# Performance work log

Measured on AMD Instinct MI355X. Metric: run time of the kernel, lower is better.

Reference implementation:

```python
import jax, jax.numpy as jnp
import numpy as np

EPS = 1.1920929e-07  # torch RMSNorm default eps = finfo(fp32).eps
NUM_HEADS = 8
UP_HEAD = 64
ROPE_HEAD = 32
TOP_K = 4
HIDDEN = 512
INTER = 256
DQ = 256
DKV = 128
N_EXPERTS = 16
B, S = 2, 2048


def _rmsnorm(x, w):
    return x * jax.lax.rsqrt(jnp.mean(x * x, axis=-1, keepdims=True) + EPS) * w


def _rope(x):
    # x: [B, h, S, D] with D = ROPE_HEAD; rotate-half RoPE, base 10000
    D = x.shape[-1]
    s = x.shape[-2]
    inv_freq = 1.0 / (10000.0 ** (jnp.arange(0, D, 2, dtype=jnp.float32) / D))
    freqs = jnp.outer(jnp.arange(s, dtype=jnp.float32), inv_freq)  # [S, D/2]
    emb = jnp.concatenate([freqs, freqs], axis=-1)  # [S, D]
    cos, sin = jnp.cos(emb), jnp.sin(emb)
    x1, x2 = x[..., : D // 2], x[..., D // 2:]
    rot = jnp.concatenate([-x2, x1], axis=-1)
    return x * cos + rot * sin


def _swiglu(x, wg, wu, wd):
    return (jax.nn.silu(x @ wg) * (x @ wu)) @ wd


def setup_inputs() -> dict:
    key = jax.random.key(0)
    ks = jax.random.split(key, 18)
    sd = 0.02
    inp = {
        "hidden_states": jax.random.normal(ks[0], (B, S, HIDDEN), jnp.float32),
        "w_in_norm": jnp.ones((HIDDEN,), jnp.float32),
        "w_dq": sd * jax.random.normal(ks[1], (HIDDEN, DQ), jnp.float32),
        "w_qnorm": jnp.ones((DQ,), jnp.float32),
        "w_uq": sd * jax.random.normal(ks[2], (DQ, NUM_HEADS * (UP_HEAD + ROPE_HEAD)), jnp.float32),
        "w_dkv": sd * jax.random.normal(ks[3], (HIDDEN, DKV + ROPE_HEAD), jnp.float32),
        "w_kvnorm": jnp.ones((DKV,), jnp.float32),
        "w_ukv": sd * jax.random.normal(ks[4], (DKV, NUM_HEADS * UP_HEAD * 2), jnp.float32),
        "w_o": sd * jax.random.normal(ks[5], (NUM_HEADS * UP_HEAD, HIDDEN), jnp.float32),
        "w_post_norm": jnp.ones((HIDDEN,), jnp.float32),
        "w_gate": sd * jax.random.normal(ks[6], (HIDDEN, N_EXPERTS), jnp.float32),
        "sh_wg": sd * jax.random.normal(ks[7], (HIDDEN, INTER), jnp.float32),
        "sh_wu": sd * jax.random.normal(ks[8], (HIDDEN, INTER), jnp.float32),
        "sh_wd": sd * jax.random.normal(ks[9], (INTER, HIDDEN), jnp.float32),
        "r_wg": sd * jax.random.normal(ks[10], (N_EXPERTS, HIDDEN, INTER), jnp.float32),
        "r_wu": sd * jax.random.normal(ks[11], (N_EXPERTS, HIDDEN, INTER), jnp.float32),
        "r_wd": sd * jax.random.normal(ks[12], (N_EXPERTS, INTER, HIDDEN), jnp.float32),
    }
    return inp


def reference(hidden_states, w_in_norm, w_dq, w_qnorm, w_uq, w_dkv, w_kvnorm,
              w_ukv, w_o, w_post_norm, w_gate, sh_wg, sh_wu, sh_wd,
              r_wg, r_wu, r_wd):
    b, s, h = hidden_states.shape
    # ---- MLA attention block ----
    residual = hidden_states
    x = _rmsnorm(hidden_states, w_in_norm)
    c_q = x @ w_dq                                             # [B,S,Dq]
    qcr = _rmsnorm(c_q, w_qnorm) @ w_uq                        # [B,S,nh*(uh+rh)]
    qcr = qcr.reshape(b, s, NUM_HEADS, UP_HEAD + ROPE_HEAD).transpose(0, 2, 1, 3)
    q_c, q_r = qcr[..., :UP_HEAD], qcr[..., UP_HEAD:]
    ckv_kr = x @ w_dkv                                         # [B,S,Dkv+rh]
    c_kv, k_r = ckv_kr[..., :DKV], ckv_kr[..., DKV:]
    k_r = k_r[:, None, :, :]                                   # [B,1,S,rh]
    kv = (_rmsnorm(c_kv, w_kvnorm) @ w_ukv).reshape(b, s, NUM_HEADS, 2 * UP_HEAD).transpose(0, 2, 1, 3)
    k_c, v = kv[..., :UP_HEAD], kv[..., UP_HEAD:]
    q = jnp.concatenate([q_c, _rope(q_r)], axis=-1)            # [B,nh,S,96]
    k = jnp.concatenate([k_c, jnp.broadcast_to(_rope(k_r), (b, NUM_HEADS, s, ROPE_HEAD))], axis=-1)
    scale = 1.0 / jnp.sqrt(jnp.float32(UP_HEAD + ROPE_HEAD))
    attn = jax.nn.softmax(jnp.einsum('bhqd,bhkd->bhqk', q, k) * scale, axis=-1)
    o = jnp.einsum('bhqk,bhkd->bhqd', attn, v).transpose(0, 2, 1, 3).reshape(b, s, NUM_HEADS * UP_HEAD)
    x = o @ w_o + residual
    # ---- MoE block ----
    residual = x
    x = _rmsnorm(x, w_post_norm)
    x2 = x.reshape(-1, h)                                      # [T,H]
    shared = _swiglu(x2, sh_wg, sh_wu, sh_wd)                  # [T,H]
    scores = jax.nn.sigmoid(x2 @ w_gate)                       # [T,E]
    tw, ti = jax.lax.top_k(scores, TOP_K)                      # [T,k]
    tw = tw / jnp.sum(tw, axis=-1, keepdims=True)
    # combine[t,e] = routing weight of expert e for token t (0 if not selected)
    combine = jnp.sum(jax.nn.one_hot(ti, N_EXPERTS, dtype=x2.dtype) * tw[..., None], axis=1)  # [T,E]
    g = jnp.einsum('th,ehi->tei', x2, r_wg)
    u = jnp.einsum('th,ehi->tei', x2, r_wu)
    y = jnp.einsum('tei,eih->teh', jax.nn.silu(g) * u, r_wd)   # per-expert SwiGLU outputs
    routed = jnp.einsum('teh,te->th', y, combine)
    return (shared + routed).reshape(b, s, h) + residual
```

## Files before the change

kernel.cpp:

```cpp
#include <hip/hip_runtime.h>
#include <hip/hip_bf16.h>
#include <math.h>

typedef float f32x4 __attribute__((ext_vector_type(4)));
typedef short s16x8 __attribute__((ext_vector_type(8)));

constexpr int Tt = 4096;
constexpr int NEn = 16;
constexpr float EPSf = 1.1920929e-07f;

__device__ __forceinline__ short f2b(float f) {
    union { __hip_bfloat16 h; short s; } u;
    u.h = __float2bfloat16(f);
    return u.s;
}
__device__ __forceinline__ float b2f(short s) {
    union { float f; unsigned u; } v;
    v.u = ((unsigned)(unsigned short)s) << 16;
    return v.f;
}

constexpr size_t alg(size_t x) { return (x + 15) & ~(size_t)15; }
constexpr size_t OFF_CQKV = 0;
constexpr size_t OFF_QCR  = alg(OFF_CQKV + (size_t)Tt * 416);
constexpr size_t OFF_KVB  = alg(OFF_QCR  + (size_t)Tt * 768);
constexpr size_t OFF_R2   = alg(OFF_KVB  + (size_t)Tt * 1024);
constexpr size_t OFF_TOKE = alg(OFF_R2   + (size_t)Tt * 512);
constexpr size_t OFF_TOKW = alg(OFF_TOKE + (size_t)Tt * 4);
constexpr size_t OFF_EWT  = alg(OFF_TOKW + (size_t)Tt * 4);
constexpr size_t OFF_ECNT = alg(OFF_EWT  + (size_t)NEn * Tt);
constexpr size_t OFF_ETOK = alg(OFF_ECNT + 64);
constexpr size_t OFF_PO   = 0;
constexpr size_t OFF_PL   = (size_t)16 * 2048 * 4 * 64 / 2;
constexpr size_t OFF_XNB   = alg(OFF_ETOK + (size_t)NEn * Tt);
constexpr size_t OFF_CQNB  = alg(OFF_XNB   + (size_t)Tt * 512 / 2);
constexpr size_t OFF_CKVNB = alg(OFF_CQNB  + (size_t)Tt * 256 / 2);
constexpr size_t OFF_QB    = alg(OFF_CKVNB + (size_t)Tt * 128 / 2);
constexpr size_t OFF_KB    = alg(OFF_QB    + (size_t)16 * 2048 * 96 / 2);
constexpr size_t OFF_VBT   = alg(OFF_KB    + (size_t)16 * 2048 * 96 / 2);
constexpr size_t OFF_XN2B  = alg(OFF_VBT   + (size_t)16 * 64 * 2048 / 2);
constexpr size_t OFF_GACT  = alg(OFF_XN2B  + (size_t)Tt * 512 / 2);
constexpr size_t OFF_EACT  = alg(OFF_GACT  + (size_t)Tt * 256 / 2);
constexpr size_t OFF_WQKVT = alg(OFF_EACT  + (size_t)16384 * 256 / 2);
constexpr size_t OFF_WUQT  = alg(OFF_WQKVT + (size_t)416 * 512 / 2);
constexpr size_t OFF_WUKVT = alg(OFF_WUQT  + (size_t)768 * 256 / 2);
constexpr size_t OFF_WOT   = alg(OFF_WUKVT + (size_t)1024 * 128 / 2);
constexpr size_t OFF_SHWGT = alg(OFF_WOT   + (size_t)512 * 512 / 2);
constexpr size_t OFF_SHWUT = alg(OFF_SHWGT + (size_t)256 * 512 / 2);
constexpr size_t OFF_SHWDT = alg(OFF_SHWUT + (size_t)256 * 512 / 2);
constexpr size_t OFF_RWGT  = alg(OFF_SHWDT + (size_t)512 * 256 / 2);
constexpr size_t OFF_RWUT  = alg(OFF_RWGT  + (size_t)16 * 256 * 512 / 2);
constexpr size_t OFF_RWDT  = alg(OFF_RWUT  + (size_t)16 * 256 * 512 / 2);

struct CvtTab {
    const float* src[11];
    short* dst[11];
    int K[11], N[11], end[11];
};
__global__ __launch_bounds__(256)
void k_cvt_all(CvtTab tab) {
    __shared__ float t[32][33];
    int bid = blockIdx.x;
    int i = 0;
    while (bid >= tab.end[i]) ++i;
    int tloc = bid - (i ? tab.end[i - 1] : 0);
    int K = tab.K[i], N = tab.N[i];
    int ntiles = N >> 5, perE = ntiles * (K >> 5);
    int e = tloc / perE, rem = tloc - e * perE;
    int k0 = (rem / ntiles) << 5, n0 = (rem % ntiles) << 5;
    size_t eo = (size_t)e * K * N;
    const float* src = tab.src[i];
    short* dst = tab.dst[i];
    int c = threadIdx.x & 31, r = threadIdx.x >> 5;
#pragma unroll
    for (int q = 0; q < 4; ++q)
        t[r + 8 * q][c] = src[eo + (size_t)(k0 + r + 8 * q) * N + n0 + c];
    __syncthreads();
#pragma unroll
    for (int q = 0; q < 4; ++q)
        dst[eo + (size_t)(n0 + r + 8 * q) * K + k0 + c] = f2b(t[c][r + 8 * q]);
}

__global__ void k_rms(const float* __restrict__ in, int inStride, const float* __restrict__ w,
                      short* __restrict__ outB, int outStride, int D, int* __restrict__ ecnt) {
    int row = blockIdx.x, tid = threadIdx.x;
    if (row == 0 && tid < 16) ecnt[tid] = 0;
    __shared__ float xs[512];
    __shared__ float red[256];
    const float* ip = in + (size_t)row * inStride;
    float ss = 0.f;
    for (int i = tid; i < D; i += 256) { float v = ip[i]; xs[i] = v; ss += v * v; }
    red[tid] = ss; __syncthreads();
    for (int s = 128; s > 0; s >>= 1) { if (tid < s) red[tid] += red[tid + s]; __syncthreads(); }
    float sc = rsqrtf(red[0] / (float)D + EPSf);
    for (int i = tid; i < D; i += 256) outB[(size_t)row * outStride + i] = f2b(xs[i] * sc * w[i]);
}

__global__ void k_rms2(const float* __restrict__ cqkv, const float* __restrict__ wq, short* __restrict__ cqnb,
                       const float* __restrict__ wkv, short* __restrict__ ckvnb) {
    int row = blockIdx.x, tid = threadIdx.x;
    __shared__ float xs[256];
    __shared__ float red[256];
    const float* ip; const float* w; short* ob; int D, outStride, r;
    if (row < Tt) { r = row;      ip = cqkv + (size_t)r * 416;       w = wq;  ob = cqnb;  D = 256; outStride = 256; }
    else          { r = row - Tt; ip = cqkv + (size_t)r * 416 + 256; w = wkv; ob = ckvnb; D = 128; outStride = 128; }
    float ss = 0.f;
    for (int i = tid; i < D; i += 256) { float v = ip[i]; xs[i] = v; ss += v * v; }
    red[tid] = ss; __syncthreads();
    for (int s = 128; s > 0; s >>= 1) { if (tid < s) red[tid] += red[tid + s]; __syncthreads(); }
    float sc = rsqrtf(red[0] / (float)D + EPSf);
    for (int i = tid; i < D; i += 256) ob[(size_t)r * outStride + i] = f2b(xs[i] * sc * w[i]);
}

__global__ __launch_bounds__(256)
void k_rms_router(const float* __restrict__ r2, const float* __restrict__ wpost,
                  const float* __restrict__ wg,
                  short* __restrict__ xn2b, int4* __restrict__ toke, float4* __restrict__ tokw) {
    int t = blockIdx.x, tid = threadIdx.x;
    __shared__ float xs[512];
    __shared__ float red[256];
    __shared__ float part[16][17];
    __shared__ float sc[16];
    const float* ip = r2 + (size_t)t * 512;
    float ss = 0.f;
    for (int i = tid; i < 512; i += 256) { float v = ip[i]; xs[i] = v; ss += v * v; }
    red[tid] = ss; __syncthreads();
    for (int s = 128; s > 0; s >>= 1) { if (tid < s) red[tid] += red[tid + s]; __syncthreads(); }
    float scale = rsqrtf(red[0] / 512.f + EPSf);
// ... 15 lines not shown
    if (tid < 16) {
        float s = 0.f;
#pragma unroll
        for (int c = 0; c < 16; ++c) s += part[c][tid];
        sc[tid] = 1.f / (1.f + expf(-s));
    }
    __syncthreads();
    if (tid < 64) {
        int lane = tid, e = lane & 15;
        float scv = sc[e];
        unsigned sel = 0;
        float tw[4]; int ti[4];
#pragma unroll
        for (int kk = 0; kk < 4; ++kk) {
            float cand = ((sel >> e) & 1u) ? -1e30f : scv;
            float mx = cand;
            mx = fmaxf(mx, __shfl_xor(mx, 1));
            mx = fmaxf(mx, __shfl_xor(mx, 2));
            mx = fmaxf(mx, __shfl_xor(mx, 4));
            mx = fmaxf(mx, __shfl_xor(mx, 8));
            unsigned long long msk = __ballot(cand == mx);
            int bi = (__ffsll(msk) - 1) & 15;
            tw[kk] = mx; ti[kk] = bi;
            sel |= 1u << bi;
        }
        if (lane == 0) {
            float inv = 1.f / (tw[0] + tw[1] + tw[2] + tw[3]);
            toke[t] = make_int4(ti[0], ti[1], ti[2], ti[3]);
            tokw[t] = make_float4(tw[0] * inv, tw[1] * inv, tw[2] * inv, tw[3] * inv);
        }
    }
}

template <int EPI>
__global__ __launch_bounds__(512)
void k_mgemm(const short* __restrict__ A, const short* __restrict__ BT,
             void* __restrict__ Cv, const float* __restrict__ add, int N, int K,
             short* __restrict__ aux, short* __restrict__ aux2) {
    __shared__ __align__(16) short As[64 * 64];
    __shared__ __align__(16) short Bs[64 * 64];
    int tid = threadIdx.x;
    int w = tid >> 6, l = tid & 63, g = l >> 4, li = l & 15;
    int wm = w >> 1, wn = w & 1;
    int m0 = blockIdx.y * 64, n0 = blockIdx.x * 64;
    f32x4 acc[2] = {};
    for (int k0 = 0; k0 < K; k0 += 64) {
        __syncthreads();
        {
            int row = tid >> 3, ch = tid & 7;
            *(int4*)&As[row * 64 + ((ch ^ (row & 7)) * 8)] =
                *(const int4*)(A + (size_t)(m0 + row) * K + k0 + 8 * ch);
            int4 v = {0, 0, 0, 0};
            if (n0 + row < N) v = *(const int4*)(BT + (size_t)(n0 + row) * K + k0 + 8 * ch);
            *(int4*)&Bs[row * 64 + ((ch ^ (row & 7)) * 8)] = v;
        }
        __syncthreads();
#pragma unroll
        for (int kc = 0; kc < 2; ++kc) {
            int row = wm * 16 + li;
            s16x8 af = *(const s16x8*)&As[row * 64 + (((4 * kc + g) ^ (li & 7)) * 8)];
#pragma unroll
            for (int nt = 0; nt < 2; ++nt) {
                int n = wn * 32 + nt * 16 + li;
                s16x8 bf = *(const s16x8*)&Bs[n * 64 + (((4 * kc + g) ^ (li & 7)) * 8)];
                acc[nt] = __builtin_amdgcn_mfma_f32_16x16x32_bf16(af, bf, acc[nt], 0, 0, 0);
            }
        }
    }
#pragma unroll
    for (int nt = 0; nt < 2; ++nt)
#pragma unroll
        for (int r = 0; r < 4; ++r) {
            int gm = m0 + wm * 16 + 4 * g + r;
            int gn = n0 + wn * 32 + nt * 16 + li;
            if (gn < N) {
                float v = acc[nt][r];
                if (EPI == 1) {
                    ((float*)Cv)[(size_t)gm * N + gn] = v + add[(size_t)gm * N + gn];
                } else if (EPI == 2) {
                    ((short*)Cv)[(size_t)gm * N + gn] = f2b(v);
                } else if (EPI == 3) {
                    int h = gn >> 7, dd = gn & 127;
                    int b = gm >> 11, srow = gm & 2047;
                    int bh = b * 8 + h;
                    if (dd < 64)
                        aux[((size_t)(bh * 2048 + srow)) * 96 + dd] = f2b(v);
                    else
                        aux2[(size_t)bh * 64 * 2048 + (size_t)(dd - 64) * 2048 + srow] = f2b(v);
                } else if (EPI == 4) {
                    int h = gn / 96, dd = gn - h * 96;
                    int b = gm >> 11, srow = gm & 2047;
                    int bh = b * 8 + h;
                    if (dd < 64)
                        aux[((size_t)(bh * 2048 + srow)) * 96 + dd] = f2b(v * 0.14724389f);
                    else
                        ((short*)Cv)[(size_t)gm * N + gn] = f2b(v);
                } else {
                    ((float*)Cv)[(size_t)gm * N + gn] = v;
                }
            }
        }
}

__global__ __launch_bounds__(512)
void k_wo_gemm(const short* __restrict__ po, const float* __restrict__ pl,
               const short* __restrict__ BT, float* __restrict__ C,
               const float* __restrict__ add) {
    constexpr int N = 512, K = 512;
    __shared__ __align__(16) short As[64 * 64];
    __shared__ __align__(16) short Bs[64 * 64];
    int tid = threadIdx.x;
    int w = tid >> 6, l = tid & 63, g = l >> 4, li = l & 15;
    int wm = w >> 1, wn = w & 1;
    int m0 = blockIdx.y * 64, n0 = blockIdx.x * 64;
    int row = tid >> 3, ch = tid & 7;
    int t = m0 + row;
    int b = t >> 11, q = t & 2047;
    f32x4 acc[2] = {};
    for (int k0 = 0; k0 < K; k0 += 64) {
        int h = k0 >> 6;
        int bhq = (b * 8 + h) * 2048 + q;
        size_t pb = (size_t)bhq * 256 + 8 * ch;
        float4 l4 = *(const float4*)(pl + (size_t)bhq * 4);
        float inv = 1.f / (l4.x + l4.y + l4.z + l4.w);
        union { int4 v; short s[8]; } p0, p1, p2, p3, ov;
        p0.v = *(const int4*)(po + pb);
        p1.v = *(const int4*)(po + pb + 64);
        p2.v = *(const int4*)(po + pb + 128);
        p3.v = *(const int4*)(po + pb + 192);
#pragma unroll
        for (int i = 0; i < 8; ++i) {
            float os = b2f(p0.s[i]) + b2f(p1.s[i]) + b2f(p2.s[i]) + b2f(p3.s[i]);
            ov.s[i] = f2b(os * inv);
        }
        int4 bv = *(const int4*)(BT + (size_t)(n0 + row) * K + k0 + 8 * ch);
        __syncthreads();
        *(int4*)&As[row * 64 + ((ch ^ (row & 7)) * 8)] = ov.v;
        *(int4*)&Bs[row * 64 + ((ch ^ (row & 7)) * 8)] = bv;
        __syncthreads();
#pragma unroll
        for (int kc = 0; kc < 2; ++kc) {
            int rr = wm * 16 + li;
            s16x8 af = *(const s16x8*)&As[rr * 64 + (((4 * kc + g) ^ (li & 7)) * 8)];
#pragma unroll
            for (int nt = 0; nt < 2; ++nt) {
                int n = wn * 32 + nt * 16 + li;
                s16x8 bf = *(const s16x8*)&Bs[n * 64 + (((4 * kc + g) ^ (li & 7)) * 8)];
                acc[nt] = __builtin_amdgcn_mfma_f32_16x16x32_bf16(af, bf, acc[nt], 0, 0, 0);
            }
        }
    }
#pragma unroll
    for (int nt = 0; nt < 2; ++nt)
#pragma unroll
        for (int r = 0; r < 4; ++r) {
            int gm = m0 + wm * 16 + 4 * g + r;
            int gn = n0 + wn * 32 + nt * 16 + li;
            C[(size_t)gm * N + gn] = acc[nt][r] + add[(size_t)gm * N + gn];
        }
}

__global__ __launch_bounds__(512)
void k_shexp(const short* __restrict__ X, const short* __restrict__ WGt, const short* __restrict__ WUt,
             short* __restrict__ gact) {
    __shared__ __align__(16) short As[64 * 64];
    __shared__ __align__(16) short Bg[64 * 64];
    __shared__ __align__(16) short Bu[64 * 64];
    int tid = threadIdx.x;
    int w = tid >> 6, l = tid & 63, g = l >> 4, li = l & 15;
    int wm = w >> 1, wn = w & 1;
    int m0 = blockIdx.x * 64, n0 = blockIdx.y * 64;
    f32x4 ag[2] = {}, au[2] = {};
    for (int k0 = 0; k0 < 512; k0 += 64) {
        __syncthreads();
        {
            int row = tid >> 3, ch = tid & 7;
            *(int4*)&As[row * 64 + ((ch ^ (row & 7)) * 8)] =
                *(const int4*)(X + (size_t)(m0 + row) * 512 + k0 + 8 * ch);
            *(int4*)&Bg[row * 64 + ((ch ^ (row & 7)) * 8)] =
                *(const int4*)(WGt + (size_t)(n0 + row) * 512 + k0 + 8 * ch);
            *(int4*)&Bu[row * 64 + ((ch ^ (row & 7)) * 8)] =
                *(const int4*)(WUt + (size_t)(n0 + row) * 512 + k0 + 8 * ch);
        }
        __syncthreads();
#pragma unroll
        for (int kc = 0; kc < 2; ++kc) {
            int row = wm * 16 + li;
            s16x8 af = *(const s16x8*)&As[row * 64 + (((4 * kc + g) ^ (li & 7)) * 8)];
#pragma unroll
            for (int nt = 0; nt < 2; ++nt) {
                int n = wn * 32 + nt * 16 + li;
                s16x8 bg = *(const s16x8*)&Bg[n * 64 + (((4 * kc + g) ^ (li & 7)) * 8)];
                s16x8 bu = *(const s16x8*)&Bu[n * 64 + (((4 * kc + g) ^ (li & 7)) * 8)];
                ag[nt] = __builtin_amdgcn_mfma_f32_16x16x32_bf16(af, bg, ag[nt], 0, 0, 0);
                au[nt] = __builtin_amdgcn_mfma_f32_16x16x32_bf16(af, bu, au[nt], 0, 0, 0);
            }
        }
    }
#pragma unroll
    for (int nt = 0; nt < 2; ++nt)
#pragma unroll
        for (int r = 0; r < 4; ++r) {
            int gm = m0 + wm * 16 + 4 * g + r;
            int gn = n0 + wn * 32 + nt * 16 + li;
            float gv = ag[nt][r], uv = au[nt][r];
            gact[(size_t)gm * 256 + gn] = f2b(gv / (1.f + __expf(-gv)) * uv);
        }
}

__global__ void k_build_rope(const short* __restrict__ qcrb, const float* __restrict__ cqkv,
                             short* __restrict__ qb, short* __restrict__ kb) {
    const float scale = 0.14724389f;
    int gid = blockIdx.x * 256 + threadIdx.x;
    const int NR = 16 * 2048 * 32;
    if (gid < NR) {
        int d2 = gid & 31;
        int rs = gid >> 5;
        int srow = rs & 2047;
        int bh = rs >> 11;
        int b = bh >> 3, h = bh & 7;
        int t = b * 2048 + srow;
        const short* src = qcrb + (size_t)t * 768 + h * 96;
        int fi = d2 & 15;
        float ang = (float)srow * __expf(-((float)(2 * fi) / 32.f) * 9.210340371976184f);
        float s, c; __sincosf(ang, &s, &c);
        float x = b2f(src[64 + d2]);
        float r = (d2 < 16) ? -b2f(src[64 + d2 + 16]) : b2f(src[64 + d2 - 16]);
        qb[((size_t)(bh * 2048 + srow)) * 96 + 64 + d2] = f2b((x * c + r * s) * scale);
    } else {
        int g2 = gid - NR;
        int d2 = g2 & 31;
        int rs = g2 >> 5;
        int srow = rs & 2047;
        int bh = rs >> 11;
        int b = bh >> 3;
        int t = b * 2048 + srow;
        int fi = d2 & 15;
        float ang = (float)srow * __expf(-((float)(2 * fi) / 32.f) * 9.210340371976184f);
        float s, c; __sincosf(ang, &s, &c);
// ... 81 lines not shown
#pragma unroll
                for (int r = 0; r < 4; ++r) { tt[r] = f2b(s[j][2 * kc][r]); tt[4 + r] = f2b(s[j][2 * kc + 1][r]); }
                pf[j][kc] = tt;
            }
#pragma unroll
        for (int dt = 0; dt < 5; ++dt) {
            int dim = dt * 16 + li;
#pragma unroll
            for (int kc = 0; kc < 2; ++kc) {
                int2 a0 = *(const int2*)&Vs[dim * 64 + (((8 * kc + g) ^ li) * 4)];
                int2 a1 = *(const int2*)&Vs[dim * 64 + (((8 * kc + 4 + g) ^ li) * 4)];
                union { s16x8 v; int i[4]; } vf;
                vf.i[0] = a0.x; vf.i[1] = a0.y; vf.i[2] = a1.x; vf.i[3] = a1.y;
                o[0][dt] = __builtin_amdgcn_mfma_f32_16x16x32_bf16(vf.v, pf[0][kc], o[0][dt], 0, 0, 0);
                o[1][dt] = __builtin_amdgcn_mfma_f32_16x16x32_bf16(vf.v, pf[1][kc], o[1][dt], 0, 0, 0);
            }
        }
    }
#pragma unroll
    for (int j = 0; j < 2; ++j) {
        int qcol = qc0 + j * 16 + li;
        size_t qbase = ((size_t)(bh * 2048 + qcol) * 4 + ks) * 64;
#pragma unroll
        for (int dt = 0; dt < 4; ++dt) {
            union { short s[4]; int2 v; } pk;
#pragma unroll
            for (int r = 0; r < 4; ++r) pk.s[r] = f2b(o[j][dt][r]);
            *(int2*)(po + qbase + dt * 16 + 4 * g) = pk.v;
        }
        if (g == 0) pl[(size_t)(bh * 2048 + qcol) * 4 + ks] = o[j][4][0];
    }
}

__global__ __launch_bounds__(256)
void k_scatter(const int4* __restrict__ toke, const float4* __restrict__ tokw,
               float* __restrict__ ewt, int* __restrict__ ecnt, int* __restrict__ etok) {
    __shared__ int lcnt[16];
    __shared__ int lbase[16];
    int tid = threadIdx.x;
    int t = blockIdx.x * 256 + tid;
    if (tid < 16) lcnt[tid] = 0;
    __syncthreads();
    int4 e4 = toke[t];
    float4 w4 = tokw[t];
    int es[4] = { e4.x, e4.y, e4.z, e4.w };
    float wv[4] = { w4.x, w4.y, w4.z, w4.w };
    int ls[4];
#pragma unroll
    for (int kk = 0; kk < 4; ++kk) ls[kk] = atomicAdd(&lcnt[es[kk]], 1);
    __syncthreads();
    if (tid < 16) lbase[tid] = atomicAdd(&ecnt[tid], lcnt[tid]);
    __syncthreads();
#pragma unroll
    for (int kk = 0; kk < 4; ++kk) {
        int slot = lbase[es[kk]] + ls[kk];
        etok[es[kk] * 4096 + slot] = t * 4 + kk;
        ewt[es[kk] * 4096 + slot] = wv[kk];
    }
}

__global__ __launch_bounds__(512)
void k_moe1m(const short* __restrict__ X, const short* __restrict__ WGt, const short* __restrict__ WUt,
             const int* __restrict__ ecnt, const int* __restrict__ etok, short* __restrict__ eact) {
    __shared__ int ecs[16];
    __shared__ __align__(16) short As[128 * 64];
    __shared__ __align__(16) short Bg[64 * 64];
    __shared__ __align__(16) short Bu[64 * 64];
    __shared__ int toks[128];
    int tid = threadIdx.x;
    if (tid < 16) ecs[tid] = ecnt[tid];
    __syncthreads();
    int lin = blockIdx.x + 144 * blockIdx.y;
    int virt = (lin & 7) * 72 + (lin >> 3);
    int bid = virt >> 2;
    int n0 = (virt & 3) * 64;
    int e = 0;
    for (; e < 16; ++e) { int n = (ecs[e] + 127) >> 7; if (bid < n) break; bid -= n; }
    if (e >= 16) return;
    int base = bid << 7;
    int rows = min(128, ecs[e] - base);
    if (tid < 128) toks[tid] = (tid < rows) ? etok[e * 4096 + base + tid] : -1;
    __syncthreads();
    int w = tid >> 6, l = tid & 63, g = l >> 4, li = l & 15;
    int wm = w >> 1, wn = w & 1;
    const short* wgp = WGt + (size_t)e * 256 * 512;
    const short* wup = WUt + (size_t)e * 256 * 512;
    f32x4 ag[2][2] = {}, au[2][2] = {};
    for (int k0 = 0; k0 < 512; k0 += 64) {
        __syncthreads();
#pragma unroll
        for (int p = 0; p < 2; ++p) {
            int flat = p * 512 + tid;
            int row = flat >> 3, ch = flat & 7;
            int tk = toks[row];
            int4 v = {0, 0, 0, 0};
            if (tk >= 0) v = *(const int4*)(X + (size_t)(tk >> 2) * 512 + k0 + 8 * ch);
            *(int4*)&As[row * 64 + ((ch ^ (row & 7)) * 8)] = v;
        }
        {
            int n = tid >> 3, ch = tid & 7;
            *(int4*)&Bg[n * 64 + ((ch ^ (n & 7)) * 8)] = *(const int4*)(wgp + (size_t)(n0 + n) * 512 + k0 + 8 * ch);
            *(int4*)&Bu[n * 64 + ((ch ^ (n & 7)) * 8)] = *(const int4*)(wup + (size_t)(n0 + n) * 512 + k0 + 8 * ch);
        }
        __syncthreads();
#pragma unroll
        for (int kc = 0; kc < 2; ++kc) {
            s16x8 af[2], bg[2], bu[2];
#pragma unroll
            for (int mt = 0; mt < 2; ++mt) {
                int row = wm * 32 + mt * 16 + li;
                af[mt] = *(const s16x8*)&As[row * 64 + (((4 * kc + g) ^ (li & 7)) * 8)];
            }
#pragma unroll
            for (int nt = 0; nt < 2; ++nt) {
                int n = wn * 32 + nt * 16 + li;
                bg[nt] = *(const s16x8*)&Bg[n * 64 + (((4 * kc + g) ^ (li & 7)) * 8)];
                bu[nt] = *(const s16x8*)&Bu[n * 64 + (((4 * kc + g) ^ (li & 7)) * 8)];
            }
#pragma unroll
            for (int mt = 0; mt < 2; ++mt)
#pragma unroll
                for (int nt = 0; nt < 2; ++nt) {
                    ag[mt][nt] = __builtin_amdgcn_mfma_f32_16x16x32_bf16(af[mt], bg[nt], ag[mt][nt], 0, 0, 0);
                    au[mt][nt] = __builtin_amdgcn_mfma_f32_16x16x32_bf16(af[mt], bu[nt], au[mt][nt], 0, 0, 0);
                }
        }
    }
#pragma unroll
    for (int mt = 0; mt < 2; ++mt)
#pragma unroll
        for (int nt = 0; nt < 2; ++nt)
#pragma unroll
            for (int r = 0; r < 4; ++r) {
                int local = wm * 32 + mt * 16 + 4 * g + r;
                if (local < rows) {
                    int entry = toks[local];
                    int gn = n0 + wn * 32 + nt * 16 + li;
                    float gv = ag[mt][nt][r], uv = au[mt][nt][r];
                    eact[(size_t)entry * 256 + gn] = f2b(gv / (1.f + __expf(-gv)) * uv);
                }
            }
}

__global__ __launch_bounds__(512)
void k_moe2m(const short* __restrict__ EA, const short* __restrict__ WDt,
             const int* __restrict__ ecnt, const int* __restrict__ etok,
             const float* __restrict__ ewt, float* __restrict__ oacc) {
    __shared__ int ecs[16];
    __shared__ __align__(16) short As[128 * 64];
    __shared__ __align__(16) short Bs[64 * 64];
    __shared__ int toks[128];
    __shared__ float wts[128];
    int tid = threadIdx.x;
    if (tid < 16) ecs[tid] = ecnt[tid];
    __syncthreads();
    int lin = blockIdx.x + 144 * blockIdx.y;
    int virt = (lin & 7) * 144 + (lin >> 3);
    int bid = virt >> 3;
    int n0 = (virt & 7) * 64;
    int e = 0;
    for (; e < 16; ++e) { int n = (ecs[e] + 127) >> 7; if (bid < n) break; bid -= n; }
    if (e >= 16) return;
    int base = bid << 7;
    int rows = min(128, ecs[e] - base);
    if (tid < 128) {
        toks[tid] = (tid < rows) ? etok[e * 4096 + base + tid] : -1;
        wts[tid]  = (tid < rows) ? ewt[e * 4096 + base + tid] : 0.f;
    }
    __syncthreads();
    int w = tid >> 6, l = tid & 63, g = l >> 4, li = l & 15;
    int wm = w >> 1, wn = w & 1;
    const short* wdp = WDt + (size_t)e * 512 * 256;
    f32x4 acc[2][2] = {};
    for (int k0 = 0; k0 < 256; k0 += 64) {
// ... 84 lines not shown
    short* ckvnb = (short*)(ws + OFF_CKVNB);
    short* qb    = (short*)(ws + OFF_QB);
    short* kb    = (short*)(ws + OFF_KB);
    short* vbt   = (short*)(ws + OFF_VBT);
    short* xn2b  = (short*)(ws + OFF_XN2B);
    short* gact  = (short*)(ws + OFF_GACT);
    short* eact  = (short*)(ws + OFF_EACT);
    short* wqkvT = (short*)(ws + OFF_WQKVT);
    short* wuqT  = (short*)(ws + OFF_WUQT);
    short* wukvT = (short*)(ws + OFF_WUKVT);
    short* woT   = (short*)(ws + OFF_WOT);
    short* shwgT = (short*)(ws + OFF_SHWGT);
    short* shwuT = (short*)(ws + OFF_SHWUT);
    short* shwdT = (short*)(ws + OFF_SHWDT);
    short* rwgT  = (short*)(ws + OFF_RWGT);
    short* rwuT  = (short*)(ws + OFF_RWUT);
    short* rwdT  = (short*)(ws + OFF_RWDT);

    float* outF = (float*)d_out;

    CvtTab tab;
    const float* srcs[11] = { w_dq, w_dkv, w_uq, w_ukv, w_o, sh_wg, sh_wu, sh_wd, r_wg, r_wu, r_wd };
    short* dsts[11] = { wqkvT, wqkvT + (size_t)256 * 512, wuqT, wukvT, woT, shwgT, shwuT, shwdT, rwgT, rwuT, rwdT };
    int Ks_[11] = { 512, 512, 256, 128, 512, 512, 512, 256, 512, 512, 256 };
    int Ns_[11] = { 256, 160, 768, 1024, 512, 256, 256, 512, 256, 256, 512 };
    int Es_[11] = { 1, 1, 1, 1, 1, 1, 1, 1, 16, 16, 16 };
    int cum = 0;
    for (int i = 0; i < 11; ++i) {
        tab.src[i] = srcs[i]; tab.dst[i] = dsts[i];
        tab.K[i] = Ks_[i]; tab.N[i] = Ns_[i];
        cum += Es_[i] * (Ks_[i] >> 5) * (Ns_[i] >> 5);
        tab.end[i] = cum;
    }
    k_cvt_all<<<cum, 256, 0, stream>>>(tab);

    k_rms<<<Tt, 256, 0, stream>>>(hs, 512, w_innorm, xnb, 512, 512, ecnt);
    k_mgemm<0><<<dim3(7, 64), 512, 0, stream>>>(xnb, wqkvT, (void*)cqkv, nullptr, 416, 512, nullptr, nullptr);
    k_rms2<<<2 * Tt, 256, 0, stream>>>(cqkv, w_qnorm, cqnb, w_kvnorm, ckvnb);
    k_mgemm<4><<<dim3(12, 64), 512, 0, stream>>>(cqnb, wuqT, (void*)qcrb, nullptr, 768, 256, qb, nullptr);
    k_mgemm<3><<<dim3(16, 64), 512, 0, stream>>>(ckvnb, wukvT, nullptr, nullptr, 1024, 128, kb, vbt);
    k_build_rope<<<(2 * 16 * 2048 * 32) / 256, 256, 0, stream>>>(qcrb, cqkv, qb, kb);
    k_attn<<<1024, 256, 0, stream>>>(qb, kb, vbt, po, pl);
    k_wo_gemm<<<dim3(8, 64), 512, 0, stream>>>(po, pl, woT, r2, hs);
    k_rms_router<<<Tt, 256, 0, stream>>>(r2, w_post, w_gate, xn2b, toke, tokw);
    k_shexp<<<dim3(64, 4), 512, 0, stream>>>(xn2b, shwgT, shwuT, gact);
    k_mgemm<1><<<dim3(8, 64), 512, 0, stream>>>(gact, shwdT, (void*)outF, r2, 512, 256, nullptr, nullptr);
    k_scatter<<<16, 256, 0, stream>>>(toke, tokw, ewt, ecnt, etok);
    k_moe1m<<<dim3(144, 4), 512, 0, stream>>>(xn2b, rwgT, rwuT, ecnt, etok, eact);
    k_moe2m<<<dim3(144, 8), 512, 0, stream>>>(eact, rwdT, ecnt, etok, ewt, outF);
}
```

Baseline: 216.0 us.

## Merge independent kernels into shared launches to cut launch count

Several independent kernels are merged into single launches that branch on block index. Weight conversion joins the input RMSNorm, the Q and KV up-projections share one grid, the shared-expert gate/up GEMM runs alongside the expert scatter, and the shared-expert down projection runs alongside the routed MoE first GEMM. This removes kernel launch gaps and lets the independent pieces fill the GPU together, at the cost of heterogeneous blocks with more register and LDS pressure per kernel.

```diff
diff --git a/kernel.cpp b/kernel.cpp
--- a/kernel.cpp
+++ b/kernel.cpp
@@ -8,6 +8,7 @@
 constexpr int Tt = 4096;
 constexpr int NEn = 16;
 constexpr float EPSf = 1.1920929e-07f;
+constexpr int CVT_BLOCKS = 7312;
 
 __device__ __forceinline__ short f2b(float f) {
     union { __hip_bfloat16 h; short s; } u;
@@ -57,43 +58,44 @@
     short* dst[11];
     int K[11], N[11], end[11];
 };
+
 __global__ __launch_bounds__(256)
-void k_cvt_all(CvtTab tab) {
+void k_cvt_rms(CvtTab tab, const float* __restrict__ in, const float* __restrict__ w,
+               short* __restrict__ outB, int* __restrict__ ecnt) {
     __shared__ float t[32][33];
-    int bid = blockIdx.x;
-    int i = 0;
-    while (bid >= tab.end[i]) ++i;
-    int tloc = bid - (i ? tab.end[i - 1] : 0);
-    int K = tab.K[i], N = tab.N[i];
-    int ntiles = N >> 5, perE = ntiles * (K >> 5);
-    int e = tloc / perE, rem = tloc - e * perE;
-    int k0 = (rem / ntiles) << 5, n0 = (rem % ntiles) << 5;
-    size_t eo = (size_t)e * K * N;
-    const float* src = tab.src[i];
-    short* dst = tab.dst[i];
-    int c = threadIdx.x & 31, r = threadIdx.x >> 5;
-#pragma unroll
-    for (int q = 0; q < 4; ++q)
-        t[r + 8 * q][c] = src[eo + (size_t)(k0 + r + 8 * q) * N + n0 + c];
-    __syncthreads();
-#pragma unroll
-    for (int q = 0; q < 4; ++q)
-        dst[eo + (size_t)(n0 + r + 8 * q) * K + k0 + c] = f2b(t[c][r + 8 * q]);
-}
-
-__global__ void k_rms(const float* __restrict__ in, int inStride, const float* __restrict__ w,
-                      short* __restrict__ outB, int outStride, int D, int* __restrict__ ecnt) {
-    int row = blockIdx.x, tid = threadIdx.x;
-    if (row == 0 && tid < 16) ecnt[tid] = 0;
     __shared__ float xs[512];
     __shared__ float red[256];
-    const float* ip = in + (size_t)row * inStride;
-    float ss = 0.f;
-    for (int i = tid; i < D; i += 256) { float v = ip[i]; xs[i] = v; ss += v * v; }
-    red[tid] = ss; __syncthreads();
-    for (int s = 128; s > 0; s >>= 1) { if (tid < s) red[tid] += red[tid + s]; __syncthreads(); }
-    float sc = rsqrtf(red[0] / (float)D + EPSf);
-    for (int i = tid; i < D; i += 256) outB[(size_t)row * outStride + i] = f2b(xs[i] * sc * w[i]);
+    int bid = blockIdx.x, tid = threadIdx.x;
+    if (bid < CVT_BLOCKS) {
+        int i = 0;
+        while (bid >= tab.end[i]) ++i;
+        int tloc = bid - (i ? tab.end[i - 1] : 0);
+        int K = tab.K[i], N = tab.N[i];
+        int ntiles = N >> 5, perE = ntiles * (K >> 5);
+        int e = tloc / perE, rem = tloc - e * perE;
+        int k0 = (rem / ntiles) << 5, n0 = (rem % ntiles) << 5;
+        size_t eo = (size_t)e * K * N;
+        const float* src = tab.src[i];
+        short* dst = tab.dst[i];
+        int c = tid & 31, r = tid >> 5;
+#pragma unroll
+        for (int q = 0; q < 4; ++q)
+            t[r + 8 * q][c] = src[eo + (size_t)(k0 + r + 8 * q) * N + n0 + c];
+        __syncthreads();
+#pragma unroll
+        for (int q = 0; q < 4; ++q)
+            dst[eo + (size_t)(n0 + r + 8 * q) * K + k0 + c] = f2b(t[c][r + 8 * q]);
+    } else {
+        int row = bid - CVT_BLOCKS;
+        if (row == 0 && tid < 16) ecnt[tid] = 0;
+        const float* ip = in + (size_t)row * 512;
+        float ss = 0.f;
+        for (int i = tid; i < 512; i += 256) { float v = ip[i]; xs[i] = v; ss += v * v; }
+        red[tid] = ss; __syncthreads();
+        for (int s = 128; s > 0; s >>= 1) { if (tid < s) red[tid] += red[tid + s]; __syncthreads(); }
+        float sc = rsqrtf(red[0] / 512.f + EPSf);
+        for (int i = tid; i < 512; i += 256) outB[(size_t)row * 512 + i] = f2b(xs[i] * sc * w[i]);
+    }
 }
 
 __global__ void k_rms2(const float* __restrict__ cqkv, const float* __restrict__ wq, short* __restrict__ cqnb,
@@ -175,11 +177,9 @@
     }
 }
 
-template <int EPI>
 __global__ __launch_bounds__(512)
-void k_mgemm(const short* __restrict__ A, const short* __restrict__ BT,
-             void* __restrict__ Cv, const float* __restrict__ add, int N, int K,
-             short* __restrict__ aux, short* __restrict__ aux2) {
+void k_mgemm0(const short* __restrict__ A, const short* __restrict__ BT,
+              float* __restrict__ C, int N, int K) {
     __shared__ __align__(16) short As[64 * 64];
     __shared__ __align__(16) short Bs[64 * 64];
     int tid = threadIdx.x;
@@ -216,31 +216,74 @@
         for (int r = 0; r < 4; ++r) {
             int gm = m0 + wm * 16 + 4 * g + r;
             int gn = n0 + wn * 32 + nt * 16 + li;
-            if (gn < N) {
-                float v = acc[nt][r];
-                if (EPI == 1) {
-                    ((float*)Cv)[(size_t)gm * N + gn] = v + add[(size_t)gm * N + gn];
-                } else if (EPI == 2) {
-                    ((short*)Cv)[(size_t)gm * N + gn] = f2b(v);
-                } else if (EPI == 3) {
-                    int h = gn >> 7, dd = gn & 127;
-                    int b = gm >> 11, srow = gm & 2047;
-                    int bh = b * 8 + h;
-                    if (dd < 64)
-                        aux[((size_t)(bh * 2048 + srow)) * 96 + dd] = f2b(v);
-                    else
-                        aux2[(size_t)bh * 64 * 2048 + (size_t)(dd - 64) * 2048 + srow] = f2b(v);
-                } else if (EPI == 4) {
-                    int h = gn / 96, dd = gn - h * 96;
-                    int b = gm >> 11, srow = gm & 2047;
-                    int bh = b * 8 + h;
-                    if (dd < 64)
-                        aux[((size_t)(bh * 2048 + srow)) * 96 + dd] = f2b(v * 0.14724389f);
-                    else
-                        ((short*)Cv)[(size_t)gm * N + gn] = f2b(v);
-                } else {
-                    ((float*)Cv)[(size_t)gm * N + gn] = v;
-                }
+            if (gn < N) C[(size_t)gm * N + gn] = acc[nt][r];
+        }
+}
+
+__global__ __launch_bounds__(512)
+void k_upproj(const short* __restrict__ cqnb, const short* __restrict__ wuqT,
+              short* __restrict__ qcrb, short* __restrict__ qb,
+              const short* __restrict__ ckvnb, const short* __restrict__ wukvT,
+              short* __restrict__ kb, short* __restrict__ vbt) {
+    __shared__ __align__(16) short As[64 * 64];
+    __shared__ __align__(16) short Bs[64 * 64];
+    int tid = threadIdx.x;
+    int w = tid >> 6, l = tid & 63, g = l >> 4, li = l & 15;
+    int wm = w >> 1, wn = w & 1;
+    bool isQ = blockIdx.x < 12;
+    const short* A  = isQ ? cqnb : ckvnb;
+    const short* BT = isQ ? wuqT : wukvT;
+    int N = isQ ? 768 : 1024;
+    int K = isQ ? 256 : 128;
+    int n0 = (isQ ? blockIdx.x : blockIdx.x - 12) * 64;
+    int m0 = blockIdx.y * 64;
+    f32x4 acc[2] = {};
+    for (int k0 = 0; k0 < K; k0 += 64) {
+        __syncthreads();
+        {
+            int row = tid >> 3, ch = tid & 7;
+            *(int4*)&As[row * 64 + ((ch ^ (row & 7)) * 8)] =
+                *(const int4*)(A + (size_t)(m0 + row) * K + k0 + 8 * ch);
+            int4 v = {0, 0, 0, 0};
+            if (n0 + row < N) v = *(const int4*)(BT + (size_t)(n0 + row) * K + k0 + 8 * ch);
+            *(int4*)&Bs[row * 64 + ((ch ^ (row & 7)) * 8)] = v;
+        }
+        __syncthreads();
+#pragma unroll
+        for (int kc = 0; kc < 2; ++kc) {
+            int row = wm * 16 + li;
+            s16x8 af = *(const s16x8*)&As[row * 64 + (((4 * kc + g) ^ (li & 7)) * 8)];
+#pragma unroll
+            for (int nt = 0; nt < 2; ++nt) {
+                int n = wn * 32 + nt * 16 + li;
+                s16x8 bf = *(const s16x8*)&Bs[n * 64 + (((4 * kc + g) ^ (li & 7)) * 8)];
+                acc[nt] = __builtin_amdgcn_mfma_f32_16x16x32_bf16(af, bf, acc[nt], 0, 0, 0);
+            }
+        }
+    }
+#pragma unroll
+    for (int nt = 0; nt < 2; ++nt)
+#pragma unroll
+        for (int r = 0; r < 4; ++r) {
+            int gm = m0 + wm * 16 + 4 * g + r;
+            int gn = n0 + wn * 32 + nt * 16 + li;
+            if (gn >= N) continue;
+            float v = acc[nt][r];
+            int b = gm >> 11, srow = gm & 2047;
+            if (isQ) {
+                int h = gn / 96, dd = gn - h * 96;
+                int bh = b * 8 + h;
+                if (dd < 64)
+                    qb[((size_t)(bh * 2048 + srow)) * 96 + dd] = f2b(v * 0.14724389f);
+                else
+                    qcrb[(size_t)gm * 768 + gn] = f2b(v);
+            } else {
+                int h = gn >> 7, dd = gn & 127;
+                int bh = b * 8 + h;
+                if (dd < 64)
+                    kb[((size_t)(bh * 2048 + srow)) * 96 + dd] = f2b(v);
+                else
+                    vbt[(size_t)bh * 64 * 2048 + (size_t)(dd - 64) * 2048 + srow] = f2b(v);
             }
         }
 }
@@ -300,54 +343,6 @@
             int gm = m0 + wm * 16 + 4 * g + r;
             int gn = n0 + wn * 32 + nt * 16 + li;
             C[(size_t)gm * N + gn] = acc[nt][r] + add[(size_t)gm * N + gn];
-        }
-}
-
-__global__ __launch_bounds__(512)
-void k_shexp(const short* __restrict__ X, const short* __restrict__ WGt, const short* __restrict__ WUt,
-             short* __restrict__ gact) {
-    __shared__ __align__(16) short As[64 * 64];
-    __shared__ __align__(16) short Bg[64 * 64];
-    __shared__ __align__(16) short Bu[64 * 64];
-    int tid = threadIdx.x;
-    int w = tid >> 6, l = tid & 63, g = l >> 4, li = l & 15;
-    int wm = w >> 1, wn = w & 1;
-    int m0 = blockIdx.x * 64, n0 = blockIdx.y * 64;
-    f32x4 ag[2] = {}, au[2] = {};
-    for (int k0 = 0; k0 < 512; k0 += 64) {
-        __syncthreads();
-        {
-            int row = tid >> 3, ch = tid & 7;
-            *(int4*)&As[row * 64 + ((ch ^ (row & 7)) * 8)] =
-                *(const int4*)(X + (size_t)(m0 + row) * 512 + k0 + 8 * ch);
-            *(int4*)&Bg[row * 64 + ((ch ^ (row & 7)) * 8)] =
-                *(const int4*)(WGt + (size_t)(n0 + row) * 512 + k0 + 8 * ch);
-            *(int4*)&Bu[row * 64 + ((ch ^ (row & 7)) * 8)] =
-                *(const int4*)(WUt + (size_t)(n0 + row) * 512 + k0 + 8 * ch);
-        }
-        __syncthreads();
-#pragma unroll
-        for (int kc = 0; kc < 2; ++kc) {
-            int row = wm * 16 + li;
-            s16x8 af = *(const s16x8*)&As[row * 64 + (((4 * kc + g) ^ (li & 7)) * 8)];
-#pragma unroll
-            for (int nt = 0; nt < 2; ++nt) {
-                int n = wn * 32 + nt * 16 + li;
-                s16x8 bg = *(const s16x8*)&Bg[n * 64 + (((4 * kc + g) ^ (li & 7)) * 8)];
-                s16x8 bu = *(const s16x8*)&Bu[n * 64 + (((4 * kc + g) ^ (li & 7)) * 8)];
-                ag[nt] = __builtin_amdgcn_mfma_f32_16x16x32_bf16(af, bg, ag[nt], 0, 0, 0);
-                au[nt] = __builtin_amdgcn_mfma_f32_16x16x32_bf16(af, bu, au[nt], 0, 0, 0);
-            }
-        }
-    }
-#pragma unroll
-    for (int nt = 0; nt < 2; ++nt)
-#pragma unroll
-        for (int r = 0; r < 4; ++r) {
-            int gm = m0 + wm * 16 + 4 * g + r;
-            int gn = n0 + wn * 32 + nt * 16 + li;
-            float gv = ag[nt][r], uv = au[nt][r];
-            gact[(size_t)gm * 256 + gn] = f2b(gv / (1.f + __expf(-gv)) * uv);
         }
 }
 
@@ -495,114 +490,210 @@
     }
 }
 
-__global__ __launch_bounds__(256)
-void k_scatter(const int4* __restrict__ toke, const float4* __restrict__ tokw,
-               float* __restrict__ ewt, int* __restrict__ ecnt, int* __restrict__ etok) {
+__global__ __launch_bounds__(512)
+void k_shexp_scatter(const short* __restrict__ X, const short* __restrict__ WGt,
+                     const short* __restrict__ WUt, short* __restrict__ gact,
+                     const int4* __restrict__ toke, const float4* __restrict__ tokw,
+                     float* __restrict__ ewt, int* __restrict__ ecnt, int* __restrict__ etok) {
+    __shared__ __align__(16) short As[64 * 64];
+    __shared__ __align__(16) short Bg[64 * 64];
+    __shared__ __align__(16) short Bu[64 * 64];
     __shared__ int lcnt[16];
     __shared__ int lbase[16];
-    int tid = threadIdx.x;
-    int t = blockIdx.x * 256 + tid;
-    if (tid < 16) lcnt[tid] = 0;
-    __syncthreads();
-    int4 e4 = toke[t];
-    float4 w4 = tokw[t];
-    int es[4] = { e4.x, e4.y, e4.z, e4.w };
-    float wv[4] = { w4.x, w4.y, w4.z, w4.w };
-    int ls[4];
-#pragma unroll
-    for (int kk = 0; kk < 4; ++kk) ls[kk] = atomicAdd(&lcnt[es[kk]], 1);
-    __syncthreads();
-    if (tid < 16) lbase[tid] = atomicAdd(&ecnt[tid], lcnt[tid]);
-    __syncthreads();
-#pragma unroll
-    for (int kk = 0; kk < 4; ++kk) {
-        int slot = lbase[es[kk]] + ls[kk];
-        etok[es[kk] * 4096 + slot] = t * 4 + kk;
-        ewt[es[kk] * 4096 + slot] = wv[kk];
+    int bid = blockIdx.x, tid = threadIdx.x;
+    if (bid < 256) {
+        int w = tid >> 6, l = tid & 63, g = l >> 4, li = l & 15;
+        int wm = w >> 1, wn = w & 1;
+        int m0 = (bid & 63) * 64, n0 = (bid >> 6) * 64;
+        f32x4 ag[2] = {}, au[2] = {};
+        for (int k0 = 0; k0 < 512; k0 += 64) {
+            __syncthreads();
+            {
+                int row = tid >> 3, ch = tid & 7;
+                *(int4*)&As[row * 64 + ((ch ^ (row & 7)) * 8)] =
+                    *(const int4*)(X + (size_t)(m0 + row) * 512 + k0 + 8 * ch);
+                *(int4*)&Bg[row * 64 + ((ch ^ (row & 7)) * 8)] =
+                    *(const int4*)(WGt + (size_t)(n0 + row) * 512 + k0 + 8 * ch);
+                *(int4*)&Bu[row * 64 + ((ch ^ (row & 7)) * 8)] =
+                    *(const int4*)(WUt + (size_t)(n0 + row) * 512 + k0 + 8 * ch);
+            }
+            __syncthreads();
+#pragma unroll
+            for (int kc = 0; kc < 2; ++kc) {
+                int row = wm * 16 + li;
+                s16x8 af = *(const s16x8*)&As[row * 64 + (((4 * kc + g) ^ (li & 7)) * 8)];
+#pragma unroll
+                for (int nt = 0; nt < 2; ++nt) {
+                    int n = wn * 32 + nt * 16 + li;
+                    s16x8 bg = *(const s16x8*)&Bg[n * 64 + (((4 * kc + g) ^ (li & 7)) * 8)];
+                    s16x8 bu = *(const s16x8*)&Bu[n * 64 + (((4 * kc + g) ^ (li & 7)) * 8)];
+                    ag[nt] = __builtin_amdgcn_mfma_f32_16x16x32_bf16(af, bg, ag[nt], 0, 0, 0);
+                    au[nt] = __builtin_amdgcn_mfma_f32_16x16x32_bf16(af, bu, au[nt], 0, 0, 0);
+                }
+            }
+        }
+#pragma unroll
+        for (int nt = 0; nt < 2; ++nt)
+#pragma unroll
+            for (int r = 0; r < 4; ++r) {
+                int gm = m0 + (tid >> 6 >> 1) * 16 + 4 * ((tid & 63) >> 4) + r;
+                int gn = n0 + ((tid >> 6) & 1) * 32 + nt * 16 + (tid & 15);
+                float gv = ag[nt][r], uv = au[nt][r];
+                gact[(size_t)gm * 256 + gn] = f2b(gv / (1.f + __expf(-gv)) * uv);
+            }
+    } else {
+        int sb = bid - 256;
+        bool act = tid < 256;
+        int t = sb * 256 + (tid & 255);
+        if (tid < 16) lcnt[tid] = 0;
+        __syncthreads();
+        int es[4]; float wv[4]; int ls[4] = {0, 0, 0, 0};
+        if (act) {
+            int4 e4 = toke[t];
+            float4 w4 = tokw[t];
+            es[0] = e4.x; es[1] = e4.y; es[2] = e4.z; es[3] = e4.w;
+            wv[0] = w4.x; wv[1] = w4.y; wv[2] = w4.z; wv[3] = w4.w;
+#pragma unroll
+            for (int kk = 0; kk < 4; ++kk) ls[kk] = atomicAdd(&lcnt[es[kk]], 1);
+        }
+        __syncthreads();
+        if (tid < 16) lbase[tid] = atomicAdd(&ecnt[tid], lcnt[tid]);
+        __syncthreads();
+        if (act) {
+#pragma unroll
+            for (int kk = 0; kk < 4; ++kk) {
+                int slot = lbase[es[kk]] + ls[kk];
+                etok[es[kk] * 4096 + slot] = t * 4 + kk;
+                ewt[es[kk] * 4096 + slot] = wv[kk];
+            }
+        }
     }
 }
 
 __global__ __launch_bounds__(512)
-void k_moe1m(const short* __restrict__ X, const short* __restrict__ WGt, const short* __restrict__ WUt,
-             const int* __restrict__ ecnt, const int* __restrict__ etok, short* __restrict__ eact) {
+void k_shd_moe1(const short* __restrict__ gact, const short* __restrict__ shwdT,
+                float* __restrict__ outF, const float* __restrict__ r2,
+                const short* __restrict__ X, const short* __restrict__ WGt,
+                const short* __restrict__ WUt,
+                const int* __restrict__ ecnt, const int* __restrict__ etok,
+                short* __restrict__ eact) {
+    __shared__ __align__(16) short smem[16384];
+    __shared__ int toks[128];
     __shared__ int ecs[16];
-    __shared__ __align__(16) short As[128 * 64];
-    __shared__ __align__(16) short Bg[64 * 64];
-    __shared__ __align__(16) short Bu[64 * 64];
-    __shared__ int toks[128];
-    int tid = threadIdx.x;
-    if (tid < 16) ecs[tid] = ecnt[tid];
-    __syncthreads();
-    int lin = blockIdx.x + 144 * blockIdx.y;
-    int virt = (lin & 7) * 72 + (lin >> 3);
-    int bid = virt >> 2;
-    int n0 = (virt & 3) * 64;
-    int e = 0;
-    for (; e < 16; ++e) { int n = (ecs[e] + 127) >> 7; if (bid < n) break; bid -= n; }
-    if (e >= 16) return;
-    int base = bid << 7;
-    int rows = min(128, ecs[e] - base);
-    if (tid < 128) toks[tid] = (tid < rows) ? etok[e * 4096 + base + tid] : -1;
-    __syncthreads();
+    int bid = blockIdx.x, tid = threadIdx.x;
     int w = tid >> 6, l = tid & 63, g = l >> 4, li = l & 15;
     int wm = w >> 1, wn = w & 1;
-    const short* wgp = WGt + (size_t)e * 256 * 512;
-    const short* wup = WUt + (size_t)e * 256 * 512;
-    f32x4 ag[2][2] = {}, au[2][2] = {};
-    for (int k0 = 0; k0 < 512; k0 += 64) {
-        __syncthreads();
-#pragma unroll
-        for (int p = 0; p < 2; ++p) {
-            int flat = p * 512 + tid;
-            int row = flat >> 3, ch = flat & 7;
-            int tk = toks[row];
-            int4 v = {0, 0, 0, 0};
-            if (tk >= 0) v = *(const int4*)(X + (size_t)(tk >> 2) * 512 + k0 + 8 * ch);
-            *(int4*)&As[row * 64 + ((ch ^ (row & 7)) * 8)] = v;
-        }
-        {
-            int n = tid >> 3, ch = tid & 7;
-            *(int4*)&Bg[n * 64 + ((ch ^ (n & 7)) * 8)] = *(const int4*)(wgp + (size_t)(n0 + n) * 512 + k0 + 8 * ch);
-            *(int4*)&Bu[n * 64 + ((ch ^ (n & 7)) * 8)] = *(const int4*)(wup + (size_t)(n0 + n) * 512 + k0 + 8 * ch);
-        }
-        __syncthreads();
-#pragma unroll
-        for (int kc = 0; kc < 2; ++kc) {
-            s16x8 af[2], bg[2], bu[2];
-#pragma unroll
-            for (int mt = 0; mt < 2; ++mt) {
-                int row = wm * 32 + mt * 16 + li;
-                af[mt] = *(const s16x8*)&As[row * 64 + (((4 * kc + g) ^ (li & 7)) * 8)];
-            }
-#pragma unroll
-            for (int nt = 0; nt < 2; ++nt) {
-                int n = wn * 32 + nt * 16 + li;
-                bg[nt] = *(const s16x8*)&Bg[n * 64 + (((4 * kc + g) ^ (li & 7)) * 8)];
-                bu[nt] = *(const s16x8*)&Bu[n * 64 + (((4 * kc + g) ^ (li & 7)) * 8)];
-            }
-#pragma unroll
-            for (int mt = 0; mt < 2; ++mt)
+    if (bid < 512) {
+        short* As = smem;
+        short* Bs = smem + 4096;
+        constexpr int N = 512, K = 256;
+        int n0 = (bid & 7) * 64, m0 = (bid >> 3) * 64;
+        f32x4 acc[2] = {};
+        for (int k0 = 0; k0 < K; k0 += 64) {
+            __syncthreads();
+            {
+                int row = tid >> 3, ch = tid & 7;
+                *(int4*)&As[row * 64 + ((ch ^ (row & 7)) * 8)] =
+                    *(const int4*)(gact + (size_t)(m0 + row) * K + k0 + 8 * ch);
+                *(int4*)&Bs[row * 64 + ((ch ^ (row & 7)) * 8)] =
+                    *(const int4*)(shwdT + (size_t)(n0 + row) * K + k0 + 8 * ch);
+            }
+            __syncthreads();
+#pragma unroll
+            for (int kc = 0; kc < 2; ++kc) {
+                int row = wm * 16 + li;
+                s16x8 af = *(const s16x8*)&As[row * 64 + (((4 * kc + g) ^ (li & 7)) * 8)];
 #pragma unroll
                 for (int nt = 0; nt < 2; ++nt) {
-                    ag[mt][nt] = __builtin_amdgcn_mfma_f32_16x16x32_bf16(af[mt], bg[nt], ag[mt][nt], 0, 0, 0);
-                    au[mt][nt] = __builtin_amdgcn_mfma_f32_16x16x32_bf16(af[mt], bu[nt], au[mt][nt], 0, 0, 0);
+                    int n = wn * 32 + nt * 16 + li;
+                    s16x8 bf = *(const s16x8*)&Bs[n * 64 + (((4 * kc + g) ^ (li & 7)) * 8)];
+                    acc[nt] = __builtin_amdgcn_mfma_f32_16x16x32_bf16(af, bf, acc[nt], 0, 0, 0);
                 }
-        }
-    }
-#pragma unroll
-    for (int mt = 0; mt < 2; ++mt)
+            }
+        }
 #pragma unroll
         for (int nt = 0; nt < 2; ++nt)
 #pragma unroll
             for (int r = 0; r < 4; ++r) {
-                int local = wm * 32 + mt * 16 + 4 * g + r;
-                if (local < rows) {
-                    int entry = toks[local];
-                    int gn = n0 + wn * 32 + nt * 16 + li;
-                    float gv = ag[mt][nt][r], uv = au[mt][nt][r];
-                    eact[(size_t)entry * 256 + gn] = f2b(gv / (1.f + __expf(-gv)) * uv);
+                int gm = m0 + wm * 16 + 4 * g + r;
+                int gn = n0 + wn * 32 + nt * 16 + li;
+                outF[(size_t)gm * N + gn] = acc[nt][r] + r2[(size_t)gm * N + gn];
+            }
+    } else {
+        short* As = smem;
+        short* Bg = smem + 8192;
+        short* Bu = smem + 12288;
+        if (tid < 16) ecs[tid] = ecnt[tid];
+        __syncthreads();
+        int lin = bid - 512;
+        int virt = (lin & 7) * 72 + (lin >> 3);
+        int tb = virt >> 2;
+        int n0 = (virt & 3) * 64;
+        int e = 0;
+        for (; e < 16; ++e) { int n = (ecs[e] + 127) >> 7; if (tb < n) break; tb -= n; }
+        if (e >= 16) return;
+        int base = tb << 7;
+        int rows = min(128, ecs[e] - base);
+        if (tid < 128) toks[tid] = (tid < rows) ? etok[e * 4096 + base + tid] : -1;
+        __syncthreads();
+        const short* wgp = WGt + (size_t)e * 256 * 512;
+        const short* wup = WUt + (size_t)e * 256 * 512;
+        f32x4 ag[2][2] = {}, au[2][2] = {};
+        for (int k0 = 0; k0 < 512; k0 += 64) {
+            __syncthreads();
+#pragma unroll
+            for (int p = 0; p < 2; ++p) {
+                int flat = p * 512 + tid;
+                int row = flat >> 3, ch = flat & 7;
+                int tk = toks[row];
+                int4 v = {0, 0, 0, 0};
+                if (tk >= 0) v = *(const int4*)(X + (size_t)(tk >> 2) * 512 + k0 + 8 * ch);
+                *(int4*)&As[row * 64 + ((ch ^ (row & 7)) * 8)] = v;
+            }
+            {
+                int n = tid >> 3, ch = tid & 7;
+                *(int4*)&Bg[n * 64 + ((ch ^ (n & 7)) * 8)] = *(const int4*)(wgp + (size_t)(n0 + n) * 512 + k0 + 8 * ch);
+                *(int4*)&Bu[n * 64 + ((ch ^ (n & 7)) * 8)] = *(const int4*)(wup + (size_t)(n0 + n) * 512 + k0 + 8 * ch);
+            }
+            __syncthreads();
+#pragma unroll
+            for (int kc = 0; kc < 2; ++kc) {
+                s16x8 af[2], bg[2], bu[2];
+#pragma unroll
+                for (int mt = 0; mt < 2; ++mt) {
+                    int row = wm * 32 + mt * 16 + li;
+                    af[mt] = *(const s16x8*)&As[row * 64 + (((4 * kc + g) ^ (li & 7)) * 8)];
                 }
-            }
+#pragma unroll
+                for (int nt = 0; nt < 2; ++nt) {
+                    int n = wn * 32 + nt * 16 + li;
+                    bg[nt] = *(const s16x8*)&Bg[n * 64 + (((4 * kc + g) ^ (li & 7)) * 8)];
+                    bu[nt] = *(const s16x8*)&Bu[n * 64 + (((4 * kc + g) ^ (li & 7)) * 8)];
+                }
+#pragma unroll
+                for (int mt = 0; mt < 2; ++mt)
+#pragma unroll
+                    for (int nt = 0; nt < 2; ++nt) {
+                        ag[mt][nt] = __builtin_amdgcn_mfma_f32_16x16x32_bf16(af[mt], bg[nt], ag[mt][nt], 0, 0, 0);
+                        au[mt][nt] = __builtin_amdgcn_mfma_f32_16x16x32_bf16(af[mt], bu[nt], au[mt][nt], 0, 0, 0);
+                    }
+            }
+        }
+#pragma unroll
+        for (int mt = 0; mt < 2; ++mt)
+#pragma unroll
+            for (int nt = 0; nt < 2; ++nt)
+#pragma unroll
+                for (int r = 0; r < 4; ++r) {
+                    int local = wm * 32 + mt * 16 + 4 * g + r;
+                    if (local < rows) {
+                        int entry = toks[local];
+                        int gn = n0 + wn * 32 + nt * 16 + li;
+                        float gv = ag[mt][nt][r], uv = au[mt][nt][r];
+                        eact[(size_t)entry * 256 + gn] = f2b(gv / (1.f + __expf(-gv)) * uv);
+                    }
+                }
+    }
 }
 
 __global__ __launch_bounds__(512)
@@ -753,20 +844,16 @@
         cum += Es_[i] * (Ks_[i] >> 5) * (Ns_[i] >> 5);
         tab.end[i] = cum;
     }
-    k_cvt_all<<<cum, 256, 0, stream>>>(tab);
-
-    k_rms<<<Tt, 256, 0, stream>>>(hs, 512, w_innorm, xnb, 512, 512, ecnt);
-    k_mgemm<0><<<dim3(7, 64), 512, 0, stream>>>(xnb, wqkvT, (void*)cqkv, nullptr, 416, 512, nullptr, nullptr);
+    k_cvt_rms<<<CVT_BLOCKS + Tt, 256, 0, stream>>>(tab, hs, w_innorm, xnb, ecnt);
+
+    k_mgemm0<<<dim3(7, 64), 512, 0, stream>>>(xnb, wqkvT, cqkv, 416, 512);
     k_rms2<<<2 * Tt, 256, 0, stream>>>(cqkv, w_qnorm, cqnb, w_kvnorm, ckvnb);
-    k_mgemm<4><<<dim3(12, 64), 512, 0, stream>>>(cqnb, wuqT, (void*)qcrb, nullptr, 768, 256, qb, nullptr);
-    k_mgemm<3><<<dim3(16, 64), 512, 0, stream>>>(ckvnb, wukvT, nullptr, nullptr, 1024, 128, kb, vbt);
+    k_upproj<<<dim3(28, 64), 512, 0, stream>>>(cqnb, wuqT, qcrb, qb, ckvnb, wukvT, kb, vbt);
     k_build_rope<<<(2 * 16 * 2048 * 32) / 256, 256, 0, stream>>>(qcrb, cqkv, qb, kb);
     k_attn<<<1024, 256, 0, stream>>>(qb, kb, vbt, po, pl);
     k_wo_gemm<<<dim3(8, 64), 512, 0, stream>>>(po, pl, woT, r2, hs);
     k_rms_router<<<Tt, 256, 0, stream>>>(r2, w_post, w_gate, xn2b, toke, tokw);
-    k_shexp<<<dim3(64, 4), 512, 0, stream>>>(xn2b, shwgT, shwuT, gact);
-    k_mgemm<1><<<dim3(8, 64), 512, 0, stream>>>(gact, shwdT, (void*)outF, r2, 512, 256, nullptr, nullptr);
-    k_scatter<<<16, 256, 0, stream>>>(toke, tokw, ewt, ecnt, etok);
-    k_moe1m<<<dim3(144, 4), 512, 0, stream>>>(xn2b, rwgT, rwuT, ecnt, etok, eact);
+    k_shexp_scatter<<<272, 512, 0, stream>>>(xn2b, shwgT, shwuT, gact, toke, tokw, ewt, ecnt, etok);
+    k_shd_moe1<<<1088, 512, 0, stream>>>(gact, shwdT, outF, r2, xn2b, rwgT, rwuT, ecnt, etok, eact);
     k_moe2m<<<dim3(144, 8), 512, 0, stream>>>(eact, rwdT, ecnt, etok, ewt, outF);
 }
```

Measured after the change: 206.2 us. 1.05x faster.
